# Performance work log

Measured on AMD Instinct MI355X. Metric: run time of the kernel, lower is better.

Reference implementation:

```python
import jax, jax.numpy as jnp
import numpy as np

D_MODEL = 1024
D_STATE = 16
D_CONV = 4
EXPAND = 2
D_INNER = D_MODEL * EXPAND


def setup_inputs() -> dict:
    key = jax.random.key(0)
    ks = jax.random.split(key, 8)
    B, L = 2, 2048
    x = jax.random.normal(ks[0], (B, L, D_MODEL), dtype=jnp.float32)
    # in_proj: Linear(d_model -> 2*d_inner), no bias
    W_in = jax.random.normal(ks[1], (D_MODEL, 2 * D_INNER), dtype=jnp.float32) / np.sqrt(D_MODEL)
    # depthwise conv1d: (d_inner, 1, d_conv) + bias
    conv_w = jax.random.normal(ks[2], (D_INNER, 1, D_CONV), dtype=jnp.float32) / np.sqrt(D_CONV)
    conv_b = jax.random.normal(ks[3], (D_INNER,), dtype=jnp.float32) * 0.01
    # x_proj: Linear(d_inner -> 2*d_state + 1), no bias
    W_x = jax.random.normal(ks[4], (D_INNER, 2 * D_STATE + 1), dtype=jnp.float32) / np.sqrt(D_INNER)
    # A_log ~ Uniform(-log(d_state), -1)
    A_log = jax.random.uniform(ks[5], (D_INNER, D_STATE), dtype=jnp.float32,
                               minval=-np.log(D_STATE), maxval=-1.0)
    D_param = jnp.ones((D_INNER,), dtype=jnp.float32)
    W_out = jax.random.normal(ks[6], (D_INNER, D_MODEL), dtype=jnp.float32) / np.sqrt(D_INNER)
    return {"x": x, "W_in": W_in, "conv_w": conv_w, "conv_b": conv_b,
            "W_x": W_x, "A_log": A_log, "D_param": D_param, "W_out": W_out}


def _selective_scan(x, delta, A, Bm, Cm):
    # x:(B,L,D), delta:(B,L), A:(D,N), Bm/Cm:(B,L,N)
    Bsz, L, Dd = x.shape
    N = A.shape[1]
    h0 = jnp.zeros((Bsz, Dd, N), dtype=x.dtype)

    def step(h, inp):
        dt, Bt, Ct, xt = inp  # (B,), wait dt:(B,), Bt:(B,N), Ct:(B,N), xt:(B,D)
        A_bar = jnp.exp(dt[:, None, None] * A)          # (B,D,N)
        dB = (dt[:, None] * Bt)[:, None, :]             # (B,1,N)
        h = A_bar * h + dB * xt[:, :, None]             # (B,D,N)
        y = jnp.einsum('bn,bdn->bd', Ct, h)             # (B,D)
        return h, y

    xs = (jnp.swapaxes(delta, 0, 1), jnp.swapaxes(Bm, 0, 1),
          jnp.swapaxes(Cm, 0, 1), jnp.swapaxes(x, 0, 1))
    _, ys = jax.lax.scan(step, h0, xs)                  # ys: (L,B,D)
    return jnp.swapaxes(ys, 0, 1)


def reference(x, W_in, conv_w, conv_b, W_x, A_log, D_param, W_out):
    B, L, _ = x.shape
    xr = x @ W_in                                       # (B,L,2*Di)
    x_inner, res = jnp.split(xr, 2, axis=-1)
    # causal depthwise conv: left-pad d_conv-1, valid conv == torch slice [:L]
    xc = jnp.swapaxes(x_inner, 1, 2)                    # (B,Di,L)
    xc = jax.lax.conv_general_dilated(
        xc, conv_w, window_strides=(1,), padding=[(D_CONV - 1, 0)],
        dimension_numbers=('NCH', 'OIH', 'NCH'), feature_group_count=D_INNER)
    xc = xc + conv_b[None, :, None]
    xc = jnp.swapaxes(xc, 1, 2)                         # (B,L,Di)
    xc = jax.nn.silu(xc)
    ssm_params = xc @ W_x                               # (B,L,1+2N)
    delta = jax.nn.softplus(ssm_params[..., 0])         # (B,L)
    Bm = ssm_params[..., 1:1 + D_STATE]                 # (B,L,N)
    Cm = ssm_params[..., 1 + D_STATE:]                  # (B,L,N)
    A = -jnp.exp(A_log)                                 # (Di,N)
    y = _selective_scan(xc, delta, A, Bm, Cm)           # (B,L,Di)
    y = y + xc * D_param[None, None, :]
    y = y * jax.nn.silu(res)
    return y @ W_out                                    # (B,L,d_model)
```

## Files before the change

### kernel.cpp

```cpp
#include <hip/hip_runtime.h>

#define L_SEQ 2048
#define NB    2
#define DMOD  1024
#define DIN   2048
#define NST   16
#define NROWS (NB*L_SEQ)
#define CL    64
#define NC    (L_SEQ/CL)

typedef unsigned short u16;
typedef _Float16 half8 __attribute__((ext_vector_type(8)));
typedef float f32x4 __attribute__((ext_vector_type(4)));
typedef short short8 __attribute__((ext_vector_type(8)));

__device__ __forceinline__ float siluf(float v){ return v / (1.f + __expf(-v)); }
__device__ __forceinline__ u16 f2h_bits(float v){ _Float16 h = (_Float16)v; return __builtin_bit_cast(u16, h); }
__device__ __forceinline__ float h2f(u16 v){ return (float)__builtin_bit_cast(_Float16, v); }
__device__ __forceinline__ float fexp2(float x){
#if __has_builtin(__builtin_amdgcn_exp2f)
    return __builtin_amdgcn_exp2f(x);
#else
    return __expf(x * 0.69314718056f);
#endif
}

__device__ __forceinline__ void gload16(const u16* g, u16* l)
{
    __builtin_amdgcn_global_load_lds(
        (const __attribute__((address_space(1))) void*)g,
        (__attribute__((address_space(3))) void*)l,
        16, 0, 0);
}

__global__ __launch_bounds__(256)
void prep_inputs(const float* __restrict__ x, const float* __restrict__ W_in,
                 const float* __restrict__ W_out, const float* __restrict__ Wx,
                 u16* __restrict__ x16, u16* __restrict__ Bt1,
                 u16* __restrict__ Bt3, u16* __restrict__ WxT16)
{
    __shared__ float s[64][65];
    const int bid = blockIdx.x, tid = threadIdx.x;
    if (bid < 4096) {
        int i = bid * 256 + tid;
        float4 v = ((const float4*)x)[i];
        ushort4 o;
        o.x = f2h_bits(v.x); o.y = f2h_bits(v.y); o.z = f2h_bits(v.z); o.w = f2h_bits(v.w);
        *(ushort4*)&x16[(size_t)i * 4] = o;
    } else if (bid < 5632) {
        const float* in; u16* outT; int R, C, rblk, cblk;
        if (bid < 5120) { int b = bid - 4096; in = W_in;  outT = Bt1; R = 1024; C = 4096; cblk = b & 63; rblk = b >> 6; }
        else            { int b = bid - 5120; in = W_out; outT = Bt3; R = 2048; C = 1024; cblk = b & 15; rblk = b >> 4; }
        int r0 = rblk * 64, c0 = cblk * 64;
        int tc = tid & 63, ty = tid >> 6;
        #pragma unroll
        for (int j = 0; j < 16; j++) {
            int r = ty + j * 4;
            s[r][tc] = in[(size_t)(r0 + r) * C + c0 + tc];
        }
        __syncthreads();
        #pragma unroll
        for (int j = 0; j < 16; j++) {
            int nn = ty + j * 4;
            outT[(size_t)(c0 + nn) * R + r0 + tc] = f2h_bits(s[tc][nn]);
        }
    } else {
        int idx = (bid - 5632) * 256 + tid;
        int n = idx >> 11, k = idx & 2047;
        float v = (n < 33) ? Wx[k * 33 + n] : 0.f;
        WxT16[idx] = f2h_bits(v);
    }
}

template<int BN, int EPI>
__global__ __launch_bounds__(256)
void gemm_mfma(const u16* __restrict__ A, const u16* __restrict__ Bt,
               void* __restrict__ C0v, void* __restrict__ C1v,
               int M, int N, int KLEN, int lda, int ldb)
{
    constexpr int NI = BN / 32;
    __shared__ __align__(16) u16 As0[128 * 64], As1[128 * 64];
    __shared__ __align__(16) u16 Bs0[BN * 64],  Bs1[BN * 64];
    const int tid  = threadIdx.x;
    const int lane = tid & 63;
    const int wid  = tid >> 6;
    const int wm   = wid >> 1, wn = wid & 1;
    const int bm = blockIdx.y * 128, bn = blockIdx.x * BN;
    const int kBase = blockIdx.z * KLEN;

    const int srow8 = lane >> 3;
    const int sunit = (lane & 7) ^ srow8;
    const u16* Ag = A  + (size_t)(bm + srow8) * lda + kBase + sunit * 8;
    const u16* Bg = Bt + (size_t)(bn + srow8) * ldb + kBase + sunit * 8;

    const int fr = lane & 15;
    const int s0 = (((lane >> 4) ^ (lane & 7))) * 8;
    const int aBase = (wm * 64 + fr) * 64 + s0;
    const int bBase = (wn * (BN / 2) + fr) * 64 + s0;

    f32x4 acc[4][NI];
    #pragma unroll
    for (int i = 0; i < 4; i++)
        #pragma unroll
        for (int j = 0; j < NI; j++)
            acc[i][j] = (f32x4){0.f, 0.f, 0.f, 0.f};

    auto STAGE = [&](u16* Ab, u16* Bb, int k0) {
        #pragma unroll
        for (int j = 0; j < 4; j++) {
            int c = wid * 4 + j;
            gload16(Ag + (size_t)(c * 8) * lda + k0, Ab + c * 512);
        }
        #pragma unroll
        for (int j = 0; j < NI; j++) {
            int c = wid * NI + j;
            gload16(Bg + (size_t)(c * 8) * ldb + k0, Bb + c * 512);
        }
    };

    auto COMPUTE = [&](const u16* Ab, const u16* Bb) {
        #pragma unroll
        for (int kk = 0; kk < 2; kk++) {
            const int x = kk ? 32 : 0;
            half8 af[4], bf[NI];
            #pragma unroll
            for (int mi = 0; mi < 4; mi++)
                af[mi] = *(const half8*)&Ab[(aBase ^ x) + mi * 1024];
            #pragma unroll
            for (int ni = 0; ni < NI; ni++)
                bf[ni] = *(const half8*)&Bb[(bBase ^ x) + ni * 1024];
            #pragma unroll
            for (int mi = 0; mi < 4; mi++)
                #pragma unroll
                for (int ni = 0; ni < NI; ni++)
                    acc[mi][ni] = __builtin_amdgcn_mfma_f32_16x16x32_f16(af[mi], bf[ni], acc[mi][ni], 0, 0, 0);
        }
    };

    const int NT = KLEN >> 6;
    STAGE(As0, Bs0, 0);
    __syncthreads();
    for (int t = 0; t < NT; t += 2) {
        if (t + 1 < NT) STAGE(As1, Bs1, (t + 1) << 6);
        COMPUTE(As0, Bs0);
        __syncthreads();
        if (t + 2 < NT) STAGE(As0, Bs0, (t + 2) << 6);
        if (t + 1 < NT) COMPUTE(As1, Bs1);
        __syncthreads();
    }

    const int cr = (lane >> 4) * 4;
    const int cc = lane & 15;
    #pragma unroll
    for (int mi = 0; mi < 4; mi++) {
        #pragma unroll
        for (int ni = 0; ni < NI; ni++) {
            #pragma unroll
            for (int q = 0; q < 4; q++) {
                int row = bm + wm * 64 + mi * 16 + cr + q;
                int col = bn + wn * (BN / 2) + ni * 16 + cc;
                float v = acc[mi][ni][q];
                if (EPI == 1) {
                    int half = N >> 1;
                    if (col < half) ((u16*)C0v)[(size_t)row * half + col] = f2h_bits(v);
                    else            ((u16*)C1v)[(size_t)row * half + col - half] = f2h_bits(siluf(v));
                } else {
                    ((u16*)C0v)[((size_t)blockIdx.z * M + row) * N + col] = f2h_bits(v);
                }
            }
        }
    }
}

__global__ __launch_bounds__(256)
void add_partials(const u16* __restrict__ p, float* __restrict__ out)
{
    int i = blockIdx.x * 256 + threadIdx.x;
    short8 a = *(const short8*)&p[(size_t)i * 8];
    short8 b = *(const short8*)&p[(size_t)NROWS * DMOD + (size_t)i * 8];
    float4 o0, o1;
    o0.x = h2f((u16)a[0]) + h2f((u16)b[0]);
    o0.y = h2f((u16)a[1]) + h2f((u16)b[1]);
    o0.z = h2f((u16)a[2]) + h2f((u16)b[2]);
    o0.w = h2f((u16)a[3]) + h2f((u16)b[3]);
    o1.x = h2f((u16)a[4]) + h2f((u16)b[4]);
    o1.y = h2f((u16)a[5]) + h2f((u16)b[5]);
    o1.z = h2f((u16)a[6]) + h2f((u16)b[6]);
    o1.w = h2f((u16)a[7]) + h2f((u16)b[7]);
    *(float4*)&out[(size_t)i * 8]     = o0;
    *(float4*)&out[(size_t)i * 8 + 4] = o1;
}

__global__ __launch_bounds__(256)
void conv_silu16(const u16* __restrict__ xin16, const float* __restrict__ cw,
                 const float* __restrict__ cb, u16* __restrict__ xc16)
{
    int idx = blockIdx.x * 256 + threadIdx.x;
    int d8 = idx & 255;
    int t  = (idx >> 8) & (L_SEQ - 1);
    int b  = idx >> 19;
    int d  = d8 << 3;
    const float4* cw4 = (const float4*)cw;
    float4 w[8];
    #pragma unroll
    for (int j = 0; j < 8; j++) w[j] = cw4[d + j];
    float acc[8];
    {
        float4 b0 = *(const float4*)&cb[d];
        float4 b1 = *(const float4*)&cb[d + 4];
        acc[0]=b0.x; acc[1]=b0.y; acc[2]=b0.z; acc[3]=b0.w;
        acc[4]=b1.x; acc[5]=b1.y; acc[6]=b1.z; acc[7]=b1.w;
    }
    #pragma unroll
    for (int k = 0; k < 4; k++) {
        int tt = t + k - 3;
        if (tt >= 0) {
            short8 v = *(const short8*)&xin16[((size_t)(b * L_SEQ + tt)) * DIN + d];
            #pragma unroll
            for (int j = 0; j < 8; j++)
                acc[j] = fmaf(h2f((u16)v[j]), (&w[j].x)[k], acc[j]);
        }
    }
    short8 o;
    #pragma unroll
    for (int j = 0; j < 8; j++) o[j] = (short)f2h_bits(siluf(acc[j]));
    *(short8*)&xc16[(size_t)idx * 8] = o;
}

__global__ __launch_bounds__(256)
void gemm2_mfma(const u16* __restrict__ A, const u16* __restrict__ Bt, float* __restrict__ pb)
{
    __shared__ __align__(16) u16 As[64 * 64];
    __shared__ __align__(16) u16 Bs[48 * 64];
    const int tid = threadIdx.x, lane = tid & 63, w = tid >> 6;
    const int bm = blockIdx.x * 64;
    const int kz = blockIdx.y;
    const int arow = tid >> 2;
    const int au   = (tid & 3) << 1;
    f32x4 acc[3];
    acc[0] = acc[1] = acc[2] = (f32x4){0.f, 0.f, 0.f, 0.f};

    for (int it = 0; it < 4; ++it) {
        const int k0 = kz * 256 + it * 64;
        short8 ra0 = *(const short8*)&A[(size_t)(bm + arow) * DIN + k0 + au * 8];
        short8 ra1 = *(const short8*)&A[(size_t)(bm + arow) * DIN + k0 + (au + 1) * 8];
        short8 rb0, rb1;
        if (tid < 192) {
            rb0 = *(const short8*)&Bt[(size_t)arow * DIN + k0 + au * 8];
            rb1 = *(const short8*)&Bt[(size_t)arow * DIN + k0 + (au + 1) * 8];
        }
        __syncthreads();
        {
            int s0 = au ^ (arow & 7), s1 = (au + 1) ^ (arow & 7);
            *(short8*)&As[arow * 64 + s0 * 8] = ra0;
            *(short8*)&As[arow * 64 + s1 * 8] = ra1;
            if (tid < 192) {
                *(short8*)&Bs[arow * 64 + s0 * 8] = rb0;
                *(short8*)&Bs[arow * 64 + s1 * 8] = rb1;
            }
        }
        __syncthreads();
        #pragma unroll
        for (int kk = 0; kk < 2; kk++) {
            int r = w * 16 + (lane & 15);
            int sl = (kk * 4 + (lane >> 4)) ^ (r & 7);
            half8 af = *(const half8*)&As[r * 64 + sl * 8];
            #pragma unroll
            for (int ni = 0; ni < 3; ni++) {
                int br = ni * 16 + (lane & 15);
                int bsl = (kk * 4 + (lane >> 4)) ^ (br & 7);
                half8 bf = *(const half8*)&Bs[br * 64 + bsl * 8];
                acc[ni] = __builtin_amdgcn_mfma_f32_16x16x32_f16(af, bf, acc[ni], 0, 0, 0);
            }
        }
    }
    #pragma unroll
    for (int ni = 0; ni < 3; ni++) {
        #pragma unroll
        for (int q = 0; q < 4; q++) {
            int row = bm + w * 16 + (lane >> 4) * 4 + q;
            int col = ni * 16 + (lane & 15);
            pb[((size_t)kz * NROWS + row) * 48 + col] = acc[ni][q];
        }
    }
}

__global__ __launch_bounds__(256)
void gemm2_reduce(const float* __restrict__ pb, float* __restrict__ delta,
                  float* __restrict__ Bm, float* __restrict__ Cm)
{
    int idx = blockIdx.x * 256 + threadIdx.x;
    int row = idx / 48, col = idx - row * 48;
    float s = 0.f;
    #pragma unroll
    for (int kz = 0; kz < 8; kz++) s += pb[(size_t)kz * NROWS * 48 + idx];
    if (col == 0)       delta[row] = fmaxf(s, 0.f) + log1pf(__expf(-fabsf(s)));
    else if (col < 17)  Bm[row * NST + col - 1]  = s;
    else if (col < 33)  Cm[row * NST + col - 17] = s;
}

__global__ __launch_bounds__(256)
void scan_part1_reg(const u16* __restrict__ xc16, const float* __restrict__ delta,
                    const float* __restrict__ Bm, const float* __restrict__ A_log,
                    float* __restrict__ h_loc, float* __restrict__ Pc)
{
    const int b = blockIdx.z, c = blockIdx.y;
    const int d = blockIdx.x * 256 + threadIdx.x;
    float ka[16];
    {
        const float4* Av = (const float4*)(A_log + (size_t)d * 16);
        #pragma unroll
        for (int q = 0; q < 4; q++) {
            float4 a = Av[q];
            ka[q*4+0] = -__expf(a.x) * 1.44269504f;
            ka[q*4+1] = -__expf(a.y) * 1.44269504f;
            ka[q*4+2] = -__expf(a.z) * 1.44269504f;
            ka[q*4+3] = -__expf(a.w) * 1.44269504f;
        }
    }
    float h[16];
    #pragma unroll
    for (int n = 0; n < 16; n++) h[n] = 0.f;
    float S = 0.f;
    const int rowbase = b * L_SEQ + c * CL;
    #pragma unroll 2
    for (int t = 0; t < CL; ++t) {
        const int rowg = rowbase + t;
        const float dt = delta[rowg];
        const float4* Bv = (const float4*)(Bm + (size_t)rowg * 16);
        float4 b0 = Bv[0], b1 = Bv[1], b2 = Bv[2], b3 = Bv[3];
        float bb[16] = {b0.x,b0.y,b0.z,b0.w, b1.x,b1.y,b1.z,b1.w,
                        b2.x,b2.y,b2.z,b2.w, b3.x,b3.y,b3.z,b3.w};
        const float xt = h2f(xc16[(size_t)rowg * DIN + d]);
        const float dtx = dt * xt;
        S += dt;
        #pragma unroll
        for (int n = 0; n < 16; n++) {
            float a = fexp2(dt * ka[n]);
            h[n] = fmaf(a, h[n], bb[n] * dtx);
        }
    }
    float* hp = h_loc + (((size_t)(b * NC + c) * DIN) + d) * 16;
    float* pp = Pc    + (((size_t)(b * NC + c) * DIN) + d) * 16;
    #pragma unroll
    for (int q = 0; q < 4; q++) {
        *(float4*)&hp[q*4] = (float4){h[q*4+0], h[q*4+1], h[q*4+2], h[q*4+3]};
        *(float4*)&pp[q*4] = (float4){fexp2(S*ka[q*4+0]), fexp2(S*ka[q*4+1]),
                                      fexp2(S*ka[q*4+2]), fexp2(S*ka[q*4+3])};
    }
}

__global__ __launch_bounds__(256)
void scan_carry(const float* __restrict__ h_loc, const float* __restrict__ Pc,
                float* __restrict__ H_in)
{
    int gid = blockIdx.x * 256 + threadIdx.x;
    int b = gid >> 15, r = gid & 32767;
    float H = 0.f;
    for (int c = 0; c < NC; ++c) {
        size_t idx = ((size_t)(b * NC + c) << 15) + r;
        H_in[idx] = H;
        H = fmaf(Pc[idx], H, h_loc[idx]);
    }
}

__global__ __launch_bounds__(256)
void scan_part3_reg(const u16* __restrict__ xc16, const float* __restrict__ delta,
                    const float* __restrict__ Bm, const float* __restrict__ Cm,
                    const float* __restrict__ A_log, const float* __restrict__ Dp,
                    const u16* __restrict__ res16, const float* __restrict__ H_in,
                    u16* __restrict__ yh)
{
    const int b = blockIdx.z, c = blockIdx.y;
    const int d = blockIdx.x * 256 + threadIdx.x;
    float ka[16];
    {
        const float4* Av = (const float4*)(A_log + (size_t)d * 16);
        #pragma unroll
        for (int q = 0; q < 4; q++) {
            float4 a = Av[q];
            ka[q*4+0] = -__expf(a.x) * 1.44269504f;
            ka[q*4+1] = -__expf(a.y) * 1.44269504f;
            ka[q*4+2] = -__expf(a.z) * 1.44269504f;
            ka[q*4+3] = -__expf(a.w) * 1.44269504f;
        }
    }
    float h[16];
    {
        const float4* Hv = (const float4*)(H_in + (((size_t)(b * NC + c) * DIN) + d) * 16);
        #pragma unroll
        for (int q = 0; q < 4; q++) {
            float4 v = Hv[q];
            h[q*4+0]=v.x; h[q*4+1]=v.y; h[q*4+2]=v.z; h[q*4+3]=v.w;
        }
    }
    const float Dpd = Dp[d];
    const int rowbase = b * L_SEQ + c * CL;
    #pragma unroll 2
    for (int t = 0; t < CL; ++t) {
        const int rowg = rowbase + t;
        const float dt = delta[rowg];
        const float4* Bv = (const float4*)(Bm + (size_t)rowg * 16);
        const float4* Cv = (const float4*)(Cm + (size_t)rowg * 16);
        float4 b0 = Bv[0], b1 = Bv[1], b2 = Bv[2], b3 = Bv[3];
        float4 c0 = Cv[0], c1 = Cv[1], c2 = Cv[2], c3 = Cv[3];
        float bb[16] = {b0.x,b0.y,b0.z,b0.w, b1.x,b1.y,b1.z,b1.w,
                        b2.x,b2.y,b2.z,b2.w, b3.x,b3.y,b3.z,b3.w};
        float cc[16] = {c0.x,c0.y,c0.z,c0.w, c1.x,c1.y,c1.z,c1.w,
                        c2.x,c2.y,c2.z,c2.w, c3.x,c3.y,c3.z,c3.w};
        const float xt = h2f(xc16[(size_t)rowg * DIN + d]);
        const float rt = h2f(res16[(size_t)rowg * DIN + d]);
        const float dtx = dt * xt;
        float y = 0.f;
        #pragma unroll
        for (int n = 0; n < 16; n++) {
            float a = fexp2(dt * ka[n]);
            h[n] = fmaf(a, h[n], bb[n] * dtx);
            y = fmaf(cc[n], h[n], y);
        }
        y = (y + xt * Dpd) * rt;
        yh[(size_t)rowg * DIN + d] = f2h_bits(y);
    }
}

extern "C" void kernel_launch(void* const* d_in, const int* in_sizes, int n_in,
                              void* d_out, int out_size, void* d_ws, size_t ws_size,
                              hipStream_t stream)
{
    const float* x     = (const float*)d_in[0];
    const float* W_in  = (const float*)d_in[1];
    const float* cw    = (const float*)d_in[2];
    const float* cb    = (const float*)d_in[3];
    const float* Wx    = (const float*)d_in[4];
    const float* A_log = (const float*)d_in[5];
    const float* Dp    = (const float*)d_in[6];
    const float* W_out = (const float*)d_in[7];
    float* out = (float*)d_out;
    float* ws  = (float*)d_ws;

    u16*   xin16 = (u16*)(ws);
    u16*   y16   = (u16*)(ws);
    u16*   res16 = (u16*)(ws + 4194304);
    u16*   xc16  = (u16*)(ws + 8388608);
    u16*   x16   = (u16*)(ws + 12582912);
    u16*   p     = (u16*)(ws + 12582912);
    u16*   Bt1   = (u16*)(ws + 14680064);
    float* pb    = ws + 14680064;
    u16*   WxT16 = (u16*)(ws + 16777216);
    float* delta = ws + 16826368;
    float* Bm    = ws + 16830464;
    float* Cm    = ws + 16896000;
    float* h_loc = ws + 16961536;
    float* Pc    = ws + 19058688;
    float* H_in  = ws + 21155840;
    u16*   Bt3   = (u16*)(ws + 23252992);

    dim3 blk(256);

    prep_inputs<<<dim3(6016), blk, 0, stream>>>(x, W_in, W_out, Wx, x16, Bt1, Bt3, WxT16);
    gemm_mfma<128, 1><<<dim3(32, 32), blk, 0, stream>>>(x16, Bt1, xin16, res16,
                                                        NROWS, 2 * DIN, DMOD, DMOD, DMOD);
    conv_silu16<<<dim3(NB * L_SEQ * (DIN / 8) / 256), blk, 0, stream>>>(xin16, cw, cb, xc16);
    gemm2_mfma<<<dim3(NROWS / 64, 8), blk, 0, stream>>>(xc16, WxT16, pb);
    gemm2_reduce<<<dim3(NROWS * 48 / 256), blk, 0, stream>>>(pb, delta, Bm, Cm);
    scan_part1_reg<<<dim3(DIN / 256, NC, NB), blk, 0, stream>>>(xc16, delta, Bm, A_log, h_loc, Pc);
    scan_carry<<<dim3(NB * DIN * NST / 256), blk, 0, stream>>>(h_loc, Pc, H_in);
    scan_part3_reg<<<dim3(DIN / 256, NC, NB), blk, 0, stream>>>(xc16, delta, Bm, Cm, A_log, Dp, res16, H_in, y16);
    gemm_mfma<128, 2><<<dim3(DMOD / 128, NROWS / 128, 2), blk, 0, stream>>>(y16, Bt3, p, nullptr,
                                                                            NROWS, DMOD, DIN / 2, DIN, DIN);
    add_partials<<<dim3(NROWS * DMOD / 8 / 256), blk, 0, stream>>>(p, out);
}
```

Before: 213.2 us.

## Pad GEMM operand leading dimensions and remap workgroups across XCDs

Pads the fp16 A/B operand row strides of both large GEMMs (1024→1056, 2048→2112) to reduce memory channel/bank conflicts from power-of-two strides. The producers (prep_inputs, scan_part3) write with the padded strides and the workspace offsets are reshuffled to fit the larger buffers. It also remaps the workgroup index so consecutive tiles land on the same XCD (stride-8 interleave) for better L2 locality. It needs more workspace and buffer aliasing changes, which could risk overlap mistakes.

```diff
diff --git a/kernel.cpp b/kernel.cpp
--- a/kernel.cpp
+++ b/kernel.cpp
@@ -8,6 +8,8 @@
 #define NROWS (NB*L_SEQ)
 #define CL    64
 #define NC    (L_SEQ/CL)
+#define LDA1  1056
+#define LDY   2112
 
 typedef unsigned short u16;
 typedef _Float16 half8 __attribute__((ext_vector_type(8)));
@@ -42,15 +44,14 @@
     __shared__ float s[64][65];
     const int bid = blockIdx.x, tid = threadIdx.x;
     if (bid < 4096) {
-        int i = bid * 256 + tid;
-        float4 v = ((const float4*)x)[i];
+        float4 v = ((const float4*)(x + (size_t)bid * DMOD))[tid];
         ushort4 o;
         o.x = f2h_bits(v.x); o.y = f2h_bits(v.y); o.z = f2h_bits(v.z); o.w = f2h_bits(v.w);
-        *(ushort4*)&x16[(size_t)i * 4] = o;
+        *(ushort4*)&x16[(size_t)bid * LDA1 + tid * 4] = o;
     } else if (bid < 5632) {
-        const float* in; u16* outT; int R, C, rblk, cblk;
-        if (bid < 5120) { int b = bid - 4096; in = W_in;  outT = Bt1; R = 1024; C = 4096; cblk = b & 63; rblk = b >> 6; }
-        else            { int b = bid - 5120; in = W_out; outT = Bt3; R = 2048; C = 1024; cblk = b & 15; rblk = b >> 4; }
+        const float* in; u16* outT; int C, ldo, rblk, cblk;
+        if (bid < 5120) { int b = bid - 4096; in = W_in;  outT = Bt1; C = 4096; ldo = LDA1; cblk = b & 63; rblk = b >> 6; }
+        else            { int b = bid - 5120; in = W_out; outT = Bt3; C = 1024; ldo = LDY;  cblk = b & 15; rblk = b >> 4; }
         int r0 = rblk * 64, c0 = cblk * 64;
         int tc = tid & 63, ty = tid >> 6;
         #pragma unroll
@@ -62,7 +63,7 @@
         #pragma unroll
         for (int j = 0; j < 16; j++) {
             int nn = ty + j * 4;
-            outT[(size_t)(c0 + nn) * R + r0 + tc] = f2h_bits(s[tc][nn]);
+            outT[(size_t)(c0 + nn) * ldo + r0 + tc] = f2h_bits(s[tc][nn]);
         }
     } else {
         int idx = (bid - 5632) * 256 + tid;
@@ -72,7 +73,7 @@
     }
 }
 
-template<int BN, int EPI>
+template<int BN, int EPI, int GX>
 __global__ __launch_bounds__(256)
 void gemm_mfma(const u16* __restrict__ A, const u16* __restrict__ Bt,
                void* __restrict__ C0v, void* __restrict__ C1v,
@@ -85,7 +86,11 @@
     const int lane = tid & 63;
     const int wid  = tid >> 6;
     const int wm   = wid >> 1, wn = wid & 1;
-    const int bm = blockIdx.y * 128, bn = blockIdx.x * BN;
+
+    const int nwg  = GX * gridDim.y;
+    const int orig = blockIdx.y * GX + blockIdx.x;
+    const int wg   = (orig & 7) * (nwg >> 3) + (orig >> 3);
+    const int bm = (wg / GX) * 128, bn = (wg % GX) * BN;
     const int kBase = blockIdx.z * KLEN;
 
     const int srow8 = lane >> 3;
@@ -419,7 +424,7 @@
             y = fmaf(cc[n], h[n], y);
         }
         y = (y + xt * Dpd) * rt;
-        yh[(size_t)rowg * DIN + d] = f2h_bits(y);
+        yh[(size_t)rowg * LDY + d] = f2h_bits(y);
     }
 }
 
@@ -440,33 +445,33 @@
 
     u16*   xin16 = (u16*)(ws);
     u16*   y16   = (u16*)(ws);
-    u16*   res16 = (u16*)(ws + 4194304);
-    u16*   xc16  = (u16*)(ws + 8388608);
-    u16*   x16   = (u16*)(ws + 12582912);
-    u16*   p     = (u16*)(ws + 12582912);
-    u16*   Bt1   = (u16*)(ws + 14680064);
-    float* pb    = ws + 14680064;
-    u16*   WxT16 = (u16*)(ws + 16777216);
-    float* delta = ws + 16826368;
-    float* Bm    = ws + 16830464;
-    float* Cm    = ws + 16896000;
-    float* h_loc = ws + 16961536;
-    float* Pc    = ws + 19058688;
-    float* H_in  = ws + 21155840;
-    u16*   Bt3   = (u16*)(ws + 23252992);
+    u16*   res16 = (u16*)(ws + 4325376);
+    u16*   xc16  = (u16*)(ws + 8519680);
+    u16*   x16   = (u16*)(ws + 12713984);
+    float* pb    = ws + 12713984;
+    u16*   Bt1   = (u16*)(ws + 14876672);
+    u16*   p     = (u16*)(ws + 14876672);
+    u16*   WxT16 = (u16*)(ws + 17039360);
+    float* delta = ws + 17088512;
+    float* Bm    = ws + 17092608;
+    float* Cm    = ws + 17158144;
+    float* h_loc = ws + 17223680;
+    float* Pc    = ws + 19320832;
+    float* H_in  = ws + 21417984;
+    u16*   Bt3   = (u16*)(ws + 23515136);
 
     dim3 blk(256);
 
     prep_inputs<<<dim3(6016), blk, 0, stream>>>(x, W_in, W_out, Wx, x16, Bt1, Bt3, WxT16);
-    gemm_mfma<128, 1><<<dim3(32, 32), blk, 0, stream>>>(x16, Bt1, xin16, res16,
-                                                        NROWS, 2 * DIN, DMOD, DMOD, DMOD);
+    gemm_mfma<128, 1, 32><<<dim3(32, 32), blk, 0, stream>>>(x16, Bt1, xin16, res16,
+                                                            NROWS, 2 * DIN, DMOD, LDA1, LDA1);
     conv_silu16<<<dim3(NB * L_SEQ * (DIN / 8) / 256), blk, 0, stream>>>(xin16, cw, cb, xc16);
     gemm2_mfma<<<dim3(NROWS / 64, 8), blk, 0, stream>>>(xc16, WxT16, pb);
     gemm2_reduce<<<dim3(NROWS * 48 / 256), blk, 0, stream>>>(pb, delta, Bm, Cm);
     scan_part1_reg<<<dim3(DIN / 256, NC, NB), blk, 0, stream>>>(xc16, delta, Bm, A_log, h_loc, Pc);
     scan_carry<<<dim3(NB * DIN * NST / 256), blk, 0, stream>>>(h_loc, Pc, H_in);
     scan_part3_reg<<<dim3(DIN / 256, NC, NB), blk, 0, stream>>>(xc16, delta, Bm, Cm, A_log, Dp, res16, H_in, y16);
-    gemm_mfma<128, 2><<<dim3(DMOD / 128, NROWS / 128, 2), blk, 0, stream>>>(y16, Bt3, p, nullptr,
-                                                                            NROWS, DMOD, DIN / 2, DIN, DIN);
+    gemm_mfma<128, 2, 8><<<dim3(DMOD / 128, NROWS / 128, 2), blk, 0, stream>>>(y16, Bt3, p, nullptr,
+                                                                               NROWS, DMOD, DIN / 2, LDY, LDY);
     add_partials<<<dim3(NROWS * DMOD / 8 / 256), blk, 0, stream>>>(p, out);
 }
```

Measured after the change: 216.1 us. Within noise of the previous version (+1.4%).

## Replace GEMM kernels with 256x256-tile 8-wave pipelined MFMA kernel, 4-way split-K

Applied to the files above, without the earlier changes.

Both large GEMMs now use a 512-thread kernel with 256x256 output tiles, double-buffered LDS filled by direct global-to-LDS loads, and interleaved partial prefetch with explicit vmcnt waits, barriers and setprio around MFMA bursts. The output projection switches from 2-way to 4-way split-K, and the partial-sum reducer now adds four fp16 slices. The workspace layout is shifted to hold the larger partial buffer. Larger tiles increase data reuse per block but cut block count (256 blocks for each GEMM), use 128KB of LDS per block, and rely on hand-placed waitcnt correctness.

```diff
diff --git a/kernel.cpp b/kernel.cpp
--- a/kernel.cpp
+++ b/kernel.cpp
@@ -32,6 +32,9 @@
         (__attribute__((address_space(3))) void*)l,
         16, 0, 0);
 }
+
+#define BARRIER() do { asm volatile("" ::: "memory"); __builtin_amdgcn_s_barrier(); asm volatile("" ::: "memory"); } while (0)
+#define VMCNT2()  asm volatile("s_waitcnt vmcnt(2)" ::: "memory")
 
 __global__ __launch_bounds__(256)
 void prep_inputs(const float* __restrict__ x, const float* __restrict__ W_in,
@@ -72,93 +75,126 @@
     }
 }
 
-template<int BN, int EPI>
-__global__ __launch_bounds__(256)
-void gemm_mfma(const u16* __restrict__ A, const u16* __restrict__ Bt,
-               void* __restrict__ C0v, void* __restrict__ C1v,
-               int M, int N, int KLEN, int lda, int ldb)
-{
-    constexpr int NI = BN / 32;
-    __shared__ __align__(16) u16 As0[128 * 64], As1[128 * 64];
-    __shared__ __align__(16) u16 Bs0[BN * 64],  Bs1[BN * 64];
+template<int EPI>
+__global__ __launch_bounds__(512, 2)
+void gemm8(const u16* __restrict__ A, const u16* __restrict__ Bt,
+           void* __restrict__ C0v, void* __restrict__ C1v,
+           int M, int N, int KLEN, int lda, int ldb)
+{
+    __shared__ __align__(16) u16 As[2 * 256 * 64];
+    __shared__ __align__(16) u16 Bs[2 * 256 * 64];
     const int tid  = threadIdx.x;
     const int lane = tid & 63;
-    const int wid  = tid >> 6;
-    const int wm   = wid >> 1, wn = wid & 1;
-    const int bm = blockIdx.y * 128, bn = blockIdx.x * BN;
+    const int w    = tid >> 6;
+    const int wm   = w >> 2, wn = w & 3;
+    const int bm = blockIdx.y * 256, bn = blockIdx.x * 256;
     const int kBase = blockIdx.z * KLEN;
 
     const int srow8 = lane >> 3;
     const int sunit = (lane & 7) ^ srow8;
     const u16* Ag = A  + (size_t)(bm + srow8) * lda + kBase + sunit * 8;
     const u16* Bg = Bt + (size_t)(bn + srow8) * ldb + kBase + sunit * 8;
-
-    const int fr = lane & 15;
-    const int s0 = (((lane >> 4) ^ (lane & 7))) * 8;
-    const int aBase = (wm * 64 + fr) * 64 + s0;
-    const int bBase = (wn * (BN / 2) + fr) * 64 + s0;
-
-    f32x4 acc[4][NI];
-    #pragma unroll
-    for (int i = 0; i < 4; i++)
-        #pragma unroll
-        for (int j = 0; j < NI; j++)
+    const int rw = w * 16;
+
+    const int fr  = lane & 15;
+    const int sl0 = ((lane >> 4) ^ (fr & 7)) * 8;
+    int aOffs[8], bOffs[4];
+    #pragma unroll
+    for (int mi = 0; mi < 8; mi++) aOffs[mi] = (wm * 128 + mi * 16 + fr) * 64 + sl0;
+    #pragma unroll
+    for (int ni = 0; ni < 4; ni++) bOffs[ni] = (ni * 64 + wn * 16 + fr) * 64 + sl0;
+
+    f32x4 acc[8][4];
+    #pragma unroll
+    for (int i = 0; i < 8; i++)
+        #pragma unroll
+        for (int j = 0; j < 4; j++)
             acc[i][j] = (f32x4){0.f, 0.f, 0.f, 0.f};
 
-    auto STAGE = [&](u16* Ab, u16* Bb, int k0) {
-        #pragma unroll
-        for (int j = 0; j < 4; j++) {
-            int c = wid * 4 + j;
-            gload16(Ag + (size_t)(c * 8) * lda + k0, Ab + c * 512);
-        }
-        #pragma unroll
-        for (int j = 0; j < NI; j++) {
-            int c = wid * NI + j;
-            gload16(Bg + (size_t)(c * 8) * ldb + k0, Bb + c * 512);
-        }
+    auto stage2 = [&](const u16* G, int ld, int rbase, int kcol, u16* ldsDst) {
+        gload16(G + (size_t)rbase * ld + kcol, ldsDst);
+        gload16(G + (size_t)(rbase + 8) * ld + kcol, ldsDst + 8 * 64);
     };
 
-    auto COMPUTE = [&](const u16* Ab, const u16* Bb) {
-        #pragma unroll
-        for (int kk = 0; kk < 2; kk++) {
-            const int x = kk ? 32 : 0;
-            half8 af[4], bf[NI];
-            #pragma unroll
-            for (int mi = 0; mi < 4; mi++)
-                af[mi] = *(const half8*)&Ab[(aBase ^ x) + mi * 1024];
-            #pragma unroll
-            for (int ni = 0; ni < NI; ni++)
-                bf[ni] = *(const half8*)&Bb[(bBase ^ x) + ni * 1024];
-            #pragma unroll
-            for (int mi = 0; mi < 4; mi++)
-                #pragma unroll
-                for (int ni = 0; ni < NI; ni++)
-                    acc[mi][ni] = __builtin_amdgcn_mfma_f32_16x16x32_f16(af[mi], bf[ni], acc[mi][ni], 0, 0, 0);
-        }
-    };
-
     const int NT = KLEN >> 6;
-    STAGE(As0, Bs0, 0);
-    __syncthreads();
-    for (int t = 0; t < NT; t += 2) {
-        if (t + 1 < NT) STAGE(As1, Bs1, (t + 1) << 6);
-        COMPUTE(As0, Bs0);
-        __syncthreads();
-        if (t + 2 < NT) STAGE(As0, Bs0, (t + 2) << 6);
-        if (t + 1 < NT) COMPUTE(As1, Bs1);
-        __syncthreads();
+    stage2(Ag, lda, 0 + rw, 0, &As[(0 + rw) * 64]);
+    stage2(Ag, lda, 128 + rw, 0, &As[(128 + rw) * 64]);
+    stage2(Bg, ldb, 0 + rw, 0, &Bs[(0 + rw) * 64]);
+    stage2(Bg, ldb, 128 + rw, 0, &Bs[(128 + rw) * 64]);
+    VMCNT2();
+    BARRIER();
+
+    for (int t = 0; t < NT; ++t) {
+        const int cO = (t & 1) << 14;
+        const int nO = cO ^ 16384;
+        const int kn = (t + 1) << 6;
+        const bool pf = (t + 1) < NT;
+        half8 af[8], bf0, bf1;
+
+        #pragma unroll
+        for (int mi = 0; mi < 8; mi++) af[mi] = *(const half8*)&As[cO + aOffs[mi]];
+        bf0 = *(const half8*)&Bs[cO + bOffs[0]];
+        bf1 = *(const half8*)&Bs[cO + bOffs[1]];
+        if (pf) stage2(Ag, lda, 0 + rw, kn, &As[nO + (0 + rw) * 64]);
+        BARRIER();
+        __builtin_amdgcn_s_setprio(1);
+        #pragma unroll
+        for (int mi = 0; mi < 8; mi++) acc[mi][0] = __builtin_amdgcn_mfma_f32_16x16x32_f16(af[mi], bf0, acc[mi][0], 0, 0, 0);
+        #pragma unroll
+        for (int mi = 0; mi < 8; mi++) acc[mi][1] = __builtin_amdgcn_mfma_f32_16x16x32_f16(af[mi], bf1, acc[mi][1], 0, 0, 0);
+        __builtin_amdgcn_s_setprio(0);
+        VMCNT2();
+        BARRIER();
+
+        bf0 = *(const half8*)&Bs[cO + bOffs[2]];
+        bf1 = *(const half8*)&Bs[cO + bOffs[3]];
+        if (pf) stage2(Ag, lda, 128 + rw, kn, &As[nO + (128 + rw) * 64]);
+        BARRIER();
+        __builtin_amdgcn_s_setprio(1);
+        #pragma unroll
+        for (int mi = 0; mi < 8; mi++) acc[mi][2] = __builtin_amdgcn_mfma_f32_16x16x32_f16(af[mi], bf0, acc[mi][2], 0, 0, 0);
+        #pragma unroll
+        for (int mi = 0; mi < 8; mi++) acc[mi][3] = __builtin_amdgcn_mfma_f32_16x16x32_f16(af[mi], bf1, acc[mi][3], 0, 0, 0);
+        __builtin_amdgcn_s_setprio(0);
+        BARRIER();
+
+        #pragma unroll
+        for (int mi = 0; mi < 8; mi++) af[mi] = *(const half8*)&As[cO + (aOffs[mi] ^ 32)];
+        bf0 = *(const half8*)&Bs[cO + (bOffs[0] ^ 32)];
+        bf1 = *(const half8*)&Bs[cO + (bOffs[1] ^ 32)];
+        if (pf) stage2(Bg, ldb, 0 + rw, kn, &Bs[nO + (0 + rw) * 64]);
+        BARRIER();
+        __builtin_amdgcn_s_setprio(1);
+        #pragma unroll
+        for (int mi = 0; mi < 8; mi++) acc[mi][0] = __builtin_amdgcn_mfma_f32_16x16x32_f16(af[mi], bf0, acc[mi][0], 0, 0, 0);
+        #pragma unroll
+        for (int mi = 0; mi < 8; mi++) acc[mi][1] = __builtin_amdgcn_mfma_f32_16x16x32_f16(af[mi], bf1, acc[mi][1], 0, 0, 0);
+        __builtin_amdgcn_s_setprio(0);
+        BARRIER();
+
+        bf0 = *(const half8*)&Bs[cO + (bOffs[2] ^ 32)];
+        bf1 = *(const half8*)&Bs[cO + (bOffs[3] ^ 32)];
+        if (pf) stage2(Bg, ldb, 128 + rw, kn, &Bs[nO + (128 + rw) * 64]);
+        BARRIER();
+        __builtin_amdgcn_s_setprio(1);
+        #pragma unroll
+        for (int mi = 0; mi < 8; mi++) acc[mi][2] = __builtin_amdgcn_mfma_f32_16x16x32_f16(af[mi], bf0, acc[mi][2], 0, 0, 0);
+        #pragma unroll
+        for (int mi = 0; mi < 8; mi++) acc[mi][3] = __builtin_amdgcn_mfma_f32_16x16x32_f16(af[mi], bf1, acc[mi][3], 0, 0, 0);
+        __builtin_amdgcn_s_setprio(0);
+        VMCNT2();
+        BARRIER();
     }
 
     const int cr = (lane >> 4) * 4;
-    const int cc = lane & 15;
-    #pragma unroll
-    for (int mi = 0; mi < 4; mi++) {
-        #pragma unroll
-        for (int ni = 0; ni < NI; ni++) {
+    #pragma unroll
+    for (int mi = 0; mi < 8; mi++) {
+        #pragma unroll
+        for (int ni = 0; ni < 4; ni++) {
             #pragma unroll
             for (int q = 0; q < 4; q++) {
-                int row = bm + wm * 64 + mi * 16 + cr + q;
-                int col = bn + wn * (BN / 2) + ni * 16 + cc;
+                int row = bm + wm * 128 + mi * 16 + cr + q;
+                int col = bn + ni * 64 + wn * 16 + fr;
                 float v = acc[mi][ni][q];
                 if (EPI == 1) {
                     int half = N >> 1;
@@ -173,20 +209,19 @@
 }
 
 __global__ __launch_bounds__(256)
-void add_partials(const u16* __restrict__ p, float* __restrict__ out)
+void add_partials4(const u16* __restrict__ p, float* __restrict__ out)
 {
     int i = blockIdx.x * 256 + threadIdx.x;
-    short8 a = *(const short8*)&p[(size_t)i * 8];
-    short8 b = *(const short8*)&p[(size_t)NROWS * DMOD + (size_t)i * 8];
-    float4 o0, o1;
-    o0.x = h2f((u16)a[0]) + h2f((u16)b[0]);
-    o0.y = h2f((u16)a[1]) + h2f((u16)b[1]);
-    o0.z = h2f((u16)a[2]) + h2f((u16)b[2]);
-    o0.w = h2f((u16)a[3]) + h2f((u16)b[3]);
-    o1.x = h2f((u16)a[4]) + h2f((u16)b[4]);
-    o1.y = h2f((u16)a[5]) + h2f((u16)b[5]);
-    o1.z = h2f((u16)a[6]) + h2f((u16)b[6]);
-    o1.w = h2f((u16)a[7]) + h2f((u16)b[7]);
+    const size_t stride = (size_t)NROWS * DMOD;
+    float acc[8] = {0,0,0,0,0,0,0,0};
+    #pragma unroll
+    for (int z = 0; z < 4; z++) {
+        short8 a = *(const short8*)&p[z * stride + (size_t)i * 8];
+        #pragma unroll
+        for (int j = 0; j < 8; j++) acc[j] += h2f((u16)a[j]);
+    }
+    float4 o0 = {acc[0], acc[1], acc[2], acc[3]};
+    float4 o1 = {acc[4], acc[5], acc[6], acc[7]};
     *(float4*)&out[(size_t)i * 8]     = o0;
     *(float4*)&out[(size_t)i * 8 + 4] = o1;
 }
@@ -443,30 +478,30 @@
     u16*   res16 = (u16*)(ws + 4194304);
     u16*   xc16  = (u16*)(ws + 8388608);
     u16*   x16   = (u16*)(ws + 12582912);
-    u16*   p     = (u16*)(ws + 12582912);
+    u16*   p4    = (u16*)(ws + 12582912);
     u16*   Bt1   = (u16*)(ws + 14680064);
     float* pb    = ws + 14680064;
-    u16*   WxT16 = (u16*)(ws + 16777216);
-    float* delta = ws + 16826368;
-    float* Bm    = ws + 16830464;
-    float* Cm    = ws + 16896000;
-    float* h_loc = ws + 16961536;
-    float* Pc    = ws + 19058688;
-    float* H_in  = ws + 21155840;
-    u16*   Bt3   = (u16*)(ws + 23252992);
-
-    dim3 blk(256);
+    u16*   WxT16 = (u16*)(ws + 20971520);
+    float* delta = ws + 21020672;
+    float* Bm    = ws + 21024768;
+    float* Cm    = ws + 21090304;
+    float* h_loc = ws + 21155840;
+    float* Pc    = ws + 23252992;
+    float* H_in  = ws + 25350144;
+    u16*   Bt3   = (u16*)(ws + 27447296);
+
+    dim3 blk(256), blk512(512);
 
     prep_inputs<<<dim3(6016), blk, 0, stream>>>(x, W_in, W_out, Wx, x16, Bt1, Bt3, WxT16);
-    gemm_mfma<128, 1><<<dim3(32, 32), blk, 0, stream>>>(x16, Bt1, xin16, res16,
-                                                        NROWS, 2 * DIN, DMOD, DMOD, DMOD);
+    gemm8<1><<<dim3(16, 16, 1), blk512, 0, stream>>>(x16, Bt1, xin16, res16,
+                                                     NROWS, 2 * DIN, DMOD, DMOD, DMOD);
     conv_silu16<<<dim3(NB * L_SEQ * (DIN / 8) / 256), blk, 0, stream>>>(xin16, cw, cb, xc16);
     gemm2_mfma<<<dim3(NROWS / 64, 8), blk, 0, stream>>>(xc16, WxT16, pb);
     gemm2_reduce<<<dim3(NROWS * 48 / 256), blk, 0, stream>>>(pb, delta, Bm, Cm);
     scan_part1_reg<<<dim3(DIN / 256, NC, NB), blk, 0, stream>>>(xc16, delta, Bm, A_log, h_loc, Pc);
     scan_carry<<<dim3(NB * DIN * NST / 256), blk, 0, stream>>>(h_loc, Pc, H_in);
     scan_part3_reg<<<dim3(DIN / 256, NC, NB), blk, 0, stream>>>(xc16, delta, Bm, Cm, A_log, Dp, res16, H_in, y16);
-    gemm_mfma<128, 2><<<dim3(DMOD / 128, NROWS / 128, 2), blk, 0, stream>>>(y16, Bt3, p, nullptr,
-                                                                            NROWS, DMOD, DIN / 2, DIN, DIN);
-    add_partials<<<dim3(NROWS * DMOD / 8 / 256), blk, 0, stream>>>(p, out);
-}
+    gemm8<2><<<dim3(DMOD / 256, NROWS / 256, 4), blk512, 0, stream>>>(y16, Bt3, p4, nullptr,
+                                                                     NROWS, DMOD, DIN / 4, DIN, DIN);
+    add_partials4<<<dim3(NROWS * DMOD / 8 / 256), blk, 0, stream>>>(p4, out);
+}
```

Result: faster. 207.3 us (-2.8%).

## Triple-buffer GEMM with K=32 stages and explicit vmcnt waits; tile conv in LDS

Applied to the files above, without the earlier changes.

Replaces the double-buffered K=64 GEMM with a triple-buffered K=32 pipeline. It uses explicit s_waitcnt vmcnt and a single barrier per step, so loads for tile t+2 overlap compute on tile t. Launch bounds are set to 3 blocks per CU to raise occupancy. The depthwise conv now stages a 35x128 tile in LDS so each time row is loaded once instead of four times. Workspace offsets are moved, and the hand-placed waitcnt counts depend on the load count per stage.

```diff
diff --git a/kernel.cpp b/kernel.cpp
--- a/kernel.cpp
+++ b/kernel.cpp
@@ -32,6 +32,10 @@
         (__attribute__((address_space(3))) void*)l,
         16, 0, 0);
 }
+
+#define BARRIER() do { asm volatile("" ::: "memory"); __builtin_amdgcn_s_barrier(); asm volatile("" ::: "memory"); } while (0)
+#define VMCNT4()  asm volatile("s_waitcnt vmcnt(4)" ::: "memory")
+#define VMCNT0()  asm volatile("s_waitcnt vmcnt(0)" ::: "memory")
 
 __global__ __launch_bounds__(256)
 void prep_inputs(const float* __restrict__ x, const float* __restrict__ W_in,
@@ -72,81 +76,76 @@
     }
 }
 
-template<int BN, int EPI>
-__global__ __launch_bounds__(256)
-void gemm_mfma(const u16* __restrict__ A, const u16* __restrict__ Bt,
-               void* __restrict__ C0v, void* __restrict__ C1v,
-               int M, int N, int KLEN, int lda, int ldb)
-{
-    constexpr int NI = BN / 32;
-    __shared__ __align__(16) u16 As0[128 * 64], As1[128 * 64];
-    __shared__ __align__(16) u16 Bs0[BN * 64],  Bs1[BN * 64];
+template<int EPI>
+__global__ __launch_bounds__(256, 3)
+void gemm97(const u16* __restrict__ A, const u16* __restrict__ Bt,
+            void* __restrict__ C0v, void* __restrict__ C1v,
+            int M, int N, int KLEN, int lda, int ldb)
+{
+    __shared__ __align__(16) u16 As[3 * 128 * 32];
+    __shared__ __align__(16) u16 Bs[3 * 128 * 32];
     const int tid  = threadIdx.x;
     const int lane = tid & 63;
     const int wid  = tid >> 6;
     const int wm   = wid >> 1, wn = wid & 1;
-    const int bm = blockIdx.y * 128, bn = blockIdx.x * BN;
+    const int bm = blockIdx.y * 128, bn = blockIdx.x * 128;
     const int kBase = blockIdx.z * KLEN;
 
-    const int srow8 = lane >> 3;
-    const int sunit = (lane & 7) ^ srow8;
-    const u16* Ag = A  + (size_t)(bm + srow8) * lda + kBase + sunit * 8;
-    const u16* Bg = Bt + (size_t)(bn + srow8) * ldb + kBase + sunit * 8;
-
-    const int fr = lane & 15;
-    const int s0 = (((lane >> 4) ^ (lane & 7))) * 8;
-    const int aBase = (wm * 64 + fr) * 64 + s0;
-    const int bBase = (wn * (BN / 2) + fr) * 64 + s0;
-
-    f32x4 acc[4][NI];
+    const int srow = lane >> 2;
+    const int g    = (lane & 3) ^ (srow & 3) ^ (lane >> 4);
+    const u16* Ag = A  + (size_t)(bm + srow) * lda + kBase + g * 8;
+    const u16* Bg = Bt + (size_t)(bn + srow) * ldb + kBase + g * 8;
+    const int c0 = wid * 2, c1 = wid * 2 + 1;
+
+    const int fr  = lane & 15;
+    const int sl0 = ((lane >> 4) ^ (fr & 3) ^ (fr >> 2)) & 3;
+    int aOff[4], bOff[4];
+    #pragma unroll
+    for (int mi = 0; mi < 4; mi++) aOff[mi] = (wm * 64 + mi * 16 + fr) * 32 + sl0 * 8;
+    #pragma unroll
+    for (int ni = 0; ni < 4; ni++) bOff[ni] = (wn * 64 + ni * 16 + fr) * 32 + sl0 * 8;
+
+    f32x4 acc[4][4];
     #pragma unroll
     for (int i = 0; i < 4; i++)
         #pragma unroll
-        for (int j = 0; j < NI; j++)
+        for (int j = 0; j < 4; j++)
             acc[i][j] = (f32x4){0.f, 0.f, 0.f, 0.f};
 
-    auto STAGE = [&](u16* Ab, u16* Bb, int k0) {
-        #pragma unroll
-        for (int j = 0; j < 4; j++) {
-            int c = wid * 4 + j;
-            gload16(Ag + (size_t)(c * 8) * lda + k0, Ab + c * 512);
-        }
-        #pragma unroll
-        for (int j = 0; j < NI; j++) {
-            int c = wid * NI + j;
-            gload16(Bg + (size_t)(c * 8) * ldb + k0, Bb + c * 512);
-        }
+    auto STAGE = [&](int t, int buf) {
+        const int kc = t * 32;
+        u16* Ad = &As[buf * 4096];
+        u16* Bd = &Bs[buf * 4096];
+        gload16(Ag + (size_t)(c0 * 16) * lda + kc, Ad + c0 * 512);
+        gload16(Ag + (size_t)(c1 * 16) * lda + kc, Ad + c1 * 512);
+        gload16(Bg + (size_t)(c0 * 16) * ldb + kc, Bd + c0 * 512);
+        gload16(Bg + (size_t)(c1 * 16) * ldb + kc, Bd + c1 * 512);
     };
 
-    auto COMPUTE = [&](const u16* Ab, const u16* Bb) {
-        #pragma unroll
-        for (int kk = 0; kk < 2; kk++) {
-            const int x = kk ? 32 : 0;
-            half8 af[4], bf[NI];
+    const int NT = KLEN >> 5;
+    STAGE(0, 0);
+    STAGE(1, 1);
+
+    int buf = 0;
+    for (int t = 0; t < NT; ++t) {
+        if (t + 1 < NT) VMCNT4(); else VMCNT0();
+        BARRIER();
+        const int bO = buf * 4096;
+        if (t + 2 < NT) {
+            int nb = buf + 2; if (nb >= 3) nb -= 3;
+            STAGE(t + 2, nb);
+        }
+        half8 af[4], bf[4];
+        #pragma unroll
+        for (int mi = 0; mi < 4; mi++) af[mi] = *(const half8*)&As[bO + aOff[mi]];
+        #pragma unroll
+        for (int ni = 0; ni < 4; ni++) bf[ni] = *(const half8*)&Bs[bO + bOff[ni]];
+        #pragma unroll
+        for (int mi = 0; mi < 4; mi++)
             #pragma unroll
-            for (int mi = 0; mi < 4; mi++)
-                af[mi] = *(const half8*)&Ab[(aBase ^ x) + mi * 1024];
-            #pragma unroll
-            for (int ni = 0; ni < NI; ni++)
-                bf[ni] = *(const half8*)&Bb[(bBase ^ x) + ni * 1024];
-            #pragma unroll
-            for (int mi = 0; mi < 4; mi++)
-                #pragma unroll
-                for (int ni = 0; ni < NI; ni++)
-                    acc[mi][ni] = __builtin_amdgcn_mfma_f32_16x16x32_f16(af[mi], bf[ni], acc[mi][ni], 0, 0, 0);
-        }
-    };
-
-    const int NT = KLEN >> 6;
-    STAGE(As0, Bs0, 0);
-    __syncthreads();
-    for (int t = 0; t < NT; t += 2) {
-        if (t + 1 < NT) STAGE(As1, Bs1, (t + 1) << 6);
-        COMPUTE(As0, Bs0);
-        __syncthreads();
-        if (t + 2 < NT) STAGE(As0, Bs0, (t + 2) << 6);
-        if (t + 1 < NT) COMPUTE(As1, Bs1);
-        __syncthreads();
+            for (int ni = 0; ni < 4; ni++)
+                acc[mi][ni] = __builtin_amdgcn_mfma_f32_16x16x32_f16(af[mi], bf[ni], acc[mi][ni], 0, 0, 0);
+        buf = (buf == 2) ? 0 : buf + 1;
     }
 
     const int cr = (lane >> 4) * 4;
@@ -154,11 +153,11 @@
     #pragma unroll
     for (int mi = 0; mi < 4; mi++) {
         #pragma unroll
-        for (int ni = 0; ni < NI; ni++) {
+        for (int ni = 0; ni < 4; ni++) {
             #pragma unroll
             for (int q = 0; q < 4; q++) {
                 int row = bm + wm * 64 + mi * 16 + cr + q;
-                int col = bn + wn * (BN / 2) + ni * 16 + cc;
+                int col = bn + wn * 64 + ni * 16 + cc;
                 float v = acc[mi][ni][q];
                 if (EPI == 1) {
                     int half = N >> 1;
@@ -192,39 +191,52 @@
 }
 
 __global__ __launch_bounds__(256)
-void conv_silu16(const u16* __restrict__ xin16, const float* __restrict__ cw,
-                 const float* __restrict__ cb, u16* __restrict__ xc16)
-{
-    int idx = blockIdx.x * 256 + threadIdx.x;
-    int d8 = idx & 255;
-    int t  = (idx >> 8) & (L_SEQ - 1);
-    int b  = idx >> 19;
-    int d  = d8 << 3;
+void conv_silu16t(const u16* __restrict__ xin16, const float* __restrict__ cw,
+                  const float* __restrict__ cb, u16* __restrict__ xc16)
+{
+    __shared__ u16 sx[35][136];
+    const int d0 = blockIdx.x << 7, t0 = blockIdx.y << 5, b = blockIdx.z;
+    const int tid = threadIdx.x;
+    for (int i = tid; i < 35 * 16; i += 256) {
+        int r = i >> 4, u = i & 15;
+        int t = t0 - 3 + r;
+        short8 v = {0,0,0,0,0,0,0,0};
+        if (t >= 0) v = *(const short8*)&xin16[((size_t)(b * L_SEQ + t)) * DIN + d0 + u * 8];
+        *(short8*)&sx[r][u * 8] = v;
+    }
+    __syncthreads();
+    const int u  = tid & 15;
+    const int tl = tid >> 4;
+    const int d  = d0 + u * 8;
     const float4* cw4 = (const float4*)cw;
     float4 w[8];
     #pragma unroll
     for (int j = 0; j < 8; j++) w[j] = cw4[d + j];
-    float acc[8];
+    float bias[8];
     {
         float4 b0 = *(const float4*)&cb[d];
         float4 b1 = *(const float4*)&cb[d + 4];
-        acc[0]=b0.x; acc[1]=b0.y; acc[2]=b0.z; acc[3]=b0.w;
-        acc[4]=b1.x; acc[5]=b1.y; acc[6]=b1.z; acc[7]=b1.w;
-    }
-    #pragma unroll
-    for (int k = 0; k < 4; k++) {
-        int tt = t + k - 3;
-        if (tt >= 0) {
-            short8 v = *(const short8*)&xin16[((size_t)(b * L_SEQ + tt)) * DIN + d];
+        bias[0]=b0.x; bias[1]=b0.y; bias[2]=b0.z; bias[3]=b0.w;
+        bias[4]=b1.x; bias[5]=b1.y; bias[6]=b1.z; bias[7]=b1.w;
+    }
+    #pragma unroll
+    for (int half = 0; half < 2; half++) {
+        const int t_l = tl + half * 16;
+        float acc[8];
+        #pragma unroll
+        for (int j = 0; j < 8; j++) acc[j] = bias[j];
+        #pragma unroll
+        for (int k = 0; k < 4; k++) {
+            short8 v = *(const short8*)&sx[t_l + k][u * 8];
             #pragma unroll
             for (int j = 0; j < 8; j++)
                 acc[j] = fmaf(h2f((u16)v[j]), (&w[j].x)[k], acc[j]);
         }
-    }
-    short8 o;
-    #pragma unroll
-    for (int j = 0; j < 8; j++) o[j] = (short)f2h_bits(siluf(acc[j]));
-    *(short8*)&xc16[(size_t)idx * 8] = o;
+        short8 o;
+        #pragma unroll
+        for (int j = 0; j < 8; j++) o[j] = (short)f2h_bits(siluf(acc[j]));
+        *(short8*)&xc16[((size_t)(b * L_SEQ + t0 + t_l)) * DIN + d] = o;
+    }
 }
 
 __global__ __launch_bounds__(256)
@@ -443,30 +455,30 @@
     u16*   res16 = (u16*)(ws + 4194304);
     u16*   xc16  = (u16*)(ws + 8388608);
     u16*   x16   = (u16*)(ws + 12582912);
-    u16*   p     = (u16*)(ws + 12582912);
+    u16*   p2    = (u16*)(ws + 12582912);
     u16*   Bt1   = (u16*)(ws + 14680064);
     float* pb    = ws + 14680064;
-    u16*   WxT16 = (u16*)(ws + 16777216);
-    float* delta = ws + 16826368;
-    float* Bm    = ws + 16830464;
-    float* Cm    = ws + 16896000;
-    float* h_loc = ws + 16961536;
-    float* Pc    = ws + 19058688;
-    float* H_in  = ws + 21155840;
-    u16*   Bt3   = (u16*)(ws + 23252992);
+    u16*   WxT16 = (u16*)(ws + 20971520);
+    float* delta = ws + 21020672;
+    float* Bm    = ws + 21024768;
+    float* Cm    = ws + 21090304;
+    float* h_loc = ws + 21155840;
+    float* Pc    = ws + 23252992;
+    float* H_in  = ws + 25350144;
+    u16*   Bt3   = (u16*)(ws + 27447296);
 
     dim3 blk(256);
 
     prep_inputs<<<dim3(6016), blk, 0, stream>>>(x, W_in, W_out, Wx, x16, Bt1, Bt3, WxT16);
-    gemm_mfma<128, 1><<<dim3(32, 32), blk, 0, stream>>>(x16, Bt1, xin16, res16,
-                                                        NROWS, 2 * DIN, DMOD, DMOD, DMOD);
-    conv_silu16<<<dim3(NB * L_SEQ * (DIN / 8) / 256), blk, 0, stream>>>(xin16, cw, cb, xc16);
+    gemm97<1><<<dim3(32, 32, 1), blk, 0, stream>>>(x16, Bt1, xin16, res16,
+                                                   NROWS, 2 * DIN, DMOD, DMOD, DMOD);
+    conv_silu16t<<<dim3(DIN / 128, L_SEQ / 32, NB), blk, 0, stream>>>(xin16, cw, cb, xc16);
     gemm2_mfma<<<dim3(NROWS / 64, 8), blk, 0, stream>>>(xc16, WxT16, pb);
     gemm2_reduce<<<dim3(NROWS * 48 / 256), blk, 0, stream>>>(pb, delta, Bm, Cm);
     scan_part1_reg<<<dim3(DIN / 256, NC, NB), blk, 0, stream>>>(xc16, delta, Bm, A_log, h_loc, Pc);
     scan_carry<<<dim3(NB * DIN * NST / 256), blk, 0, stream>>>(h_loc, Pc, H_in);
     scan_part3_reg<<<dim3(DIN / 256, NC, NB), blk, 0, stream>>>(xc16, delta, Bm, Cm, A_log, Dp, res16, H_in, y16);
-    gemm_mfma<128, 2><<<dim3(DMOD / 128, NROWS / 128, 2), blk, 0, stream>>>(y16, Bt3, p, nullptr,
-                                                                            NROWS, DMOD, DIN / 2, DIN, DIN);
-    add_partials<<<dim3(NROWS * DMOD / 8 / 256), blk, 0, stream>>>(p, out);
-}
+    gemm97<2><<<dim3(DMOD / 128, NROWS / 128, 2), blk, 0, stream>>>(y16, Bt3, p2, nullptr,
+                                                                   NROWS, DMOD, DIN / 2, DIN, DIN);
+    add_partials<<<dim3(NROWS * DMOD / 8 / 256), blk, 0, stream>>>(p2, out);
+}
```

New measurement: 204.0 us. 1.05x faster.
